# Optimization experiments

Hardware: AMD Instinct MI355X
Metric: run time of the kernel (lower is better)

Reference implementation:

```python
import jax, jax.numpy as jnp
import numpy as np

N, E, K, DEG = 150_000, 3_000_000, 4, 2
S = K * K  # 16 kernel weight matrices (kernel_size=4, dim=2)


def spline_coeffs(edge_attr):
    """Open quadratic B-spline basis, dim=2, kernel_size=4.
    Returns C [E, 16]: per-edge coefficient for each kernel weight index."""
    u = jnp.clip(edge_attr, 0.0, 1.0)
    v = u * (K - DEG)                      # [E,2], in [0, K-DEG]
    kv = jnp.floor(v)
    t = v - kv                             # [E,2] fractional part
    # quadratic uniform B-spline pieces
    b = jnp.stack([0.5 * (1.0 - t) ** 2,
                   -t * t + t + 0.5,
                   0.5 * t * t], axis=-1)  # [E,2,3]
    idx = jnp.clip(kv[..., None].astype(jnp.int32) + jnp.arange(3), 0, K - 1)  # [E,2,3]
    basis = (b[:, 0, :, None] * b[:, 1, None, :]).reshape(-1, 9)               # [E,9]
    widx = (idx[:, 0, :, None] + K * idx[:, 1, None, :]).reshape(-1, 9)        # [E,9]
    e_ar = jnp.arange(widx.shape[0])[:, None]
    C = jnp.zeros((widx.shape[0], S), basis.dtype).at[e_ar, widx].add(basis)   # [E,16]
    return C


def spline_conv(x, src, dst, C, weight, root, bias):
    # out_i = sum_{e: dst=i} sum_k C[e,k] * x[src[e]] @ W[k]  + x_i @ root + bias
    x_j = x[src]                                              # [E, in] gather
    out = x @ root + bias                                     # root_weight + bias
    for k in range(S):  # static small loop over 16 kernel matrices
        agg = jax.ops.segment_sum(C[:, k:k + 1] * x_j, dst, num_segments=N)  # [N,in]
        out = out + agg @ weight[k]
    return out


def batch_norm(x, gamma, beta, eps=1e-5):
    m = x.mean(axis=0)
    v = x.var(axis=0)  # biased, as torch BatchNorm1d training forward
    return (x - m) * jax.lax.rsqrt(v + eps) * gamma + beta


def setup_inputs() -> dict:
    key = jax.random.key(0)
    ks = jax.random.split(key, 18)
    f32 = jnp.float32
    return {
        "x": jax.random.normal(ks[0], (N, 1), f32),
        "edge_index": jax.random.randint(ks[1], (2, E), 0, N),
        "edge_attr": jax.random.uniform(ks[2], (E, 2), f32),
        "w1": jax.random.normal(ks[3], (S, 1, 32), f32) * 0.25,
        "root1": jax.random.normal(ks[4], (1, 32), f32) * 0.25,
        "b1": jnp.zeros((32,), f32),
        "gamma1": jnp.ones((32,), f32),
        "beta1": jnp.zeros((32,), f32),
        "w2": jax.random.normal(ks[5], (S, 32, 64), f32) * 0.05,
        "root2": jax.random.normal(ks[6], (32, 64), f32) * 0.05,
        "b2": jnp.zeros((64,), f32),
        "gamma2": jnp.ones((64,), f32),
        "beta2": jnp.zeros((64,), f32),
        "fc1_w": jax.random.normal(ks[7], (64, 128), f32) * 0.1,
        "fc1_b": jnp.zeros((128,), f32),
        "fc2_w": jax.random.normal(ks[8], (128, 1), f32) * 0.1,
        "fc2_b": jnp.zeros((1,), f32),
    }


def reference(x, edge_index, edge_attr, w1, root1, b1, gamma1, beta1,
              w2, root2, b2, gamma2, beta2, fc1_w, fc1_b, fc2_w, fc2_b):
    src, dst = edge_index[0], edge_index[1]
    C = spline_coeffs(edge_attr)            # shared by both conv layers
    h = spline_conv(x, src, dst, C, w1, root1, b1)
    h = jax.nn.elu(batch_norm(h, gamma1, beta1))
    h = spline_conv(h, src, dst, C, w2, root2, b2)
    h = jax.nn.elu(batch_norm(h, gamma2, beta2))  # [N,64]; flatten is identity
    h = jax.nn.elu(h @ fc1_w + fc1_b)
    return h @ fc2_w + fc2_b                 # [N,1]
```

## Files before the change

kernel.cpp:

```cpp
#include <hip/hip_runtime.h>
#include <hip/hip_fp16.h>
#include <math.h>


typedef _Float16 half8 __attribute__((ext_vector_type(8)));
typedef _Float16 half4 __attribute__((ext_vector_type(4)));
typedef float    f32x4 __attribute__((ext_vector_type(4)));
typedef int      iv4   __attribute__((ext_vector_type(4)));

#define ACHUNK 8192

__device__ __forceinline__ void bspline4(float a, float B[4]) {
    a = fminf(fmaxf(a, 0.f), 1.f);
    float v  = a * 2.0f;
    float kv = floorf(v);
    float t  = v - kv;
    int   ik = (int)kv;
    float b0 = 0.5f * (1.f - t) * (1.f - t);
    float b1 = (t - t * t) + 0.5f;
    float b2 = 0.5f * t * t;
    int c0 = ik;
    int c1 = ik + 1;
    int c2 = ik + 2; if (c2 > 3) c2 = 3;
#pragma unroll
    for (int j = 0; j < 4; ++j)
        B[j] = (c0 == j ? b0 : 0.f) + (c1 == j ? b1 : 0.f) + (c2 == j ? b2 : 0.f);
}

__device__ __forceinline__ float eluf(float x) {
    return x > 0.f ? x : expm1f(x);
}

__device__ __forceinline__ void unpack_basis(uint4 rec, float bu[4], float bv[4]) {
    float2 f01 = __half22float2(*(const __half2*)&rec.y);
    float2 f23 = __half22float2(*(const __half2*)&rec.z);
    float2 f45 = __half22float2(*(const __half2*)&rec.w);
    bu[0] = f01.x; bu[1] = f01.y; bu[2] = f23.x;
    bu[3] = 1.f - (bu[0] + bu[1] + bu[2]);
    bv[0] = f23.y; bv[1] = f45.x; bv[2] = f45.y;
    bv[3] = 1.f - (bv[0] + bv[1] + bv[2]);
}

__device__ __forceinline__ uint4 make_edge_rec(unsigned src, float u, float v) {
    float Bu[4], Bv[4];
    bspline4(u, Bu);
    bspline4(v, Bv);
    __half2 p01 = __floats2half2_rn(Bu[0], Bu[1]);
    __half2 p23 = __floats2half2_rn(Bu[2], Bv[0]);
    __half2 p45 = __floats2half2_rn(Bv[1], Bv[2]);
    uint4 rec;
    rec.x = src;
    rec.y = *(const unsigned*)&p01;
    rec.z = *(const unsigned*)&p23;
    rec.w = *(const unsigned*)&p45;
    return rec;
}


__global__ void kA1_hist(const int* __restrict__ dst, int E, int* __restrict__ cnt,
                         int nWG, int NBUK) {
    extern __shared__ int hist[];
    int wg = blockIdx.x, tid = threadIdx.x;
    for (int b = tid; b < NBUK; b += 256) hist[b] = 0;
    __syncthreads();
    int base = wg * ACHUNK;
    int end  = base + ACHUNK; if (end > E) end = E;
    for (int i = base + tid; i < end; i += 256)
        atomicAdd(&hist[dst[i] >> 8], 1);
    __syncthreads();
    for (int b = tid; b < NBUK; b += 256) cnt[b * nWG + wg] = hist[b];
}

__global__ void k_scan1(const int* __restrict__ in, int M,
                        int* __restrict__ outp, int* __restrict__ blockSums) {
    __shared__ int wsum[4];
    int tid  = threadIdx.x;
    int base = blockIdx.x * 1024 + tid * 4;
    int d0 = (base + 0) < M ? in[base + 0] : 0;
    int d1 = (base + 1) < M ? in[base + 1] : 0;
    int d2 = (base + 2) < M ? in[base + 2] : 0;
    int d3 = (base + 3) < M ? in[base + 3] : 0;
    int s4 = d0 + d1 + d2 + d3;
    int lane = tid & 63, wid = tid >> 6;
    int inc = s4;
#pragma unroll
    for (int off = 1; off < 64; off <<= 1) {
        int t = __shfl_up(inc, off);
        if (lane >= off) inc += t;
    }
    if (lane == 63) wsum[wid] = inc;
    __syncthreads();
    if (tid == 0) {
        int acc = 0;
#pragma unroll
        for (int w = 0; w < 4; ++w) { int t = wsum[w]; wsum[w] = acc; acc += t; }
    }
    __syncthreads();
    int ebase = wsum[wid] + inc - s4;
    if ((base + 0) < M) outp[base + 0] = ebase;
    if ((base + 1) < M) outp[base + 1] = ebase + d0;
    if ((base + 2) < M) outp[base + 2] = ebase + d0 + d1;
    if ((base + 3) < M) outp[base + 3] = ebase + d0 + d1 + d2;
    if (tid == 255) blockSums[blockIdx.x] = ebase + s4;
}

__global__ void k_scan2(const int* __restrict__ blockSums, int NB, int* __restrict__ blockOff) {
    __shared__ int sh[256];
    int tid = threadIdx.x;
    int own = (tid < NB) ? blockSums[tid] : 0;
    sh[tid] = own;
    __syncthreads();
    for (int off = 1; off < 256; off <<= 1) {
        int v = (tid >= off) ? sh[tid - off] : 0;
        __syncthreads();
        sh[tid] += v;
        __syncthreads();
    }
    if (tid < NB) blockOff[tid] = sh[tid] - own;
}

__global__ void k_scan3b(int* __restrict__ arr, const int* __restrict__ blockOff, int M) {
    int i = blockIdx.x * blockDim.x + threadIdx.x;
    if (i < M) arr[i] += blockOff[i >> 10];
}

__global__ __launch_bounds__(256) void kA2_fill(
    const int* __restrict__ ei, const float* __restrict__ attr, int E,
    const int* __restrict__ offs, int nWG, int NBUK,
    uint4* __restrict__ buf1, unsigned char* __restrict__ dl1) {
    extern __shared__ int lds[];
    int*            hist  = lds;
    int*            pref  = hist + NBUK;
    unsigned short* s2e   = (unsigned short*)(pref + NBUK);
    unsigned short* bslot = s2e + ACHUNK;
    __shared__ int wsum[4];
    int wg = blockIdx.x, tid = threadIdx.x;
    int base  = wg * ACHUNK;
    int csize = E - base; if (csize > ACHUNK) csize = ACHUNK;

    for (int b = tid; b < NBUK; b += 256) hist[b] = 0;
    __syncthreads();

    int ranks[32];
#pragma unroll
    for (int k = 0; k < 32; ++k) {
        int i = tid + (k << 8);
        if (i < csize) {
            int b = ei[E + base + i] >> 8;
            ranks[k] = atomicAdd(&hist[b], 1);
        }
    }
    __syncthreads();

    int IT = (NBUK + 255) >> 8;
    int b0 = tid * IT;
    int lsum = 0;
    for (int k = 0; k < IT; ++k) {
        int b = b0 + k;
        if (b < NBUK) lsum += hist[b];
    }
    int lane = tid & 63, wid = tid >> 6;
    int inc = lsum;
#pragma unroll
    for (int off = 1; off < 64; off <<= 1) {
        int t = __shfl_up(inc, off);
        if (lane >= off) inc += t;
    }
    if (lane == 63) wsum[wid] = inc;
    __syncthreads();
    if (tid == 0) {
        int acc = 0;
#pragma unroll
        for (int w = 0; w < 4; ++w) { int t = wsum[w]; wsum[w] = acc; acc += t; }
    }
    __syncthreads();
    int run = wsum[wid] + inc - lsum;
    for (int k = 0; k < IT; ++k) {
        int b = b0 + k;
        if (b < NBUK) { pref[b] = run; run += hist[b]; }
    }
    __syncthreads();

#pragma unroll
    for (int k = 0; k < 32; ++k) {
        int i = tid + (k << 8);
        if (i < csize) {
            int b = ei[E + base + i] >> 8;
            int s = pref[b] + ranks[k];
            s2e[s]   = (unsigned short)i;
            bslot[s] = (unsigned short)b;
        }
    }
    __syncthreads();

    for (int s = tid; s < csize; s += 256) {
        int i  = s2e[s];
        int b  = bslot[s];
        int gi = base + i;
        int gpos = offs[b * nWG + wg] + (s - pref[b]);
        int d  = ei[E + gi];
        uint4 rec = make_edge_rec((unsigned)ei[gi], attr[2 * gi], attr[2 * gi + 1]);
        buf1[gpos] = rec;
        dl1[gpos]  = (unsigned char)(d & 255);
    }
}


__global__ __launch_bounds__(256) void kB_sort(
    const uint4* __restrict__ buf1, const unsigned char* __restrict__ dl1,
    const int* __restrict__ off, int nWG, int NBUK, int N, int E,
    uint4* __restrict__ edges, int* __restrict__ rowptr) {
    __shared__ int hist[256], pref[256], curs[256];
    __shared__ int sbase, ssize;
    int b = blockIdx.x, tid = threadIdx.x;
    if (tid == 0) {
        int s  = off[b * nWG];
        int e2 = (b + 1 < NBUK) ? off[(b + 1) * nWG] : E;
        sbase = s; ssize = e2 - s;
    }
    hist[tid] = 0;
    __syncthreads();
    int base = sbase, size = ssize;
    for (int i = tid; i < size; i += 256) atomicAdd(&hist[dl1[base + i]], 1);
    __syncthreads();
    if (tid == 0) {
        int acc = 0;
        for (int j = 0; j < 256; ++j) { pref[j] = acc; acc += hist[j]; }
    }
    __syncthreads();
    curs[tid] = pref[tid];
    int node = b * 256 + tid;
    if (node < N) rowptr[node] = base + pref[tid];
    if (b == NBUK - 1 && tid == 0) rowptr[N] = E;
    __syncthreads();
    for (int i = tid; i < size; i += 256) {
        int p = atomicAdd(&curs[dl1[base + i]], 1);
        edges[base + p] = buf1[base + i];
    }
}


__global__ void k_w2pack(const float* __restrict__ w2, const float* __restrict__ root2,
                         _Float16* __restrict__ w2f) {
    int f = blockIdx.x * blockDim.x + threadIdx.x;
    int stride = gridDim.x * blockDim.x;
    for (; f < 34816; f += stride) {
        int j = f & 7, l = (f >> 3) & 63, t = (f >> 9) & 3;
        int o = t * 16 + (l & 15);
        float v;
        if (f < 32768) {
            int s = f >> 11;
            int p = s * 32 + ((l >> 4) << 3) + j;
            int ch = p >> 4, k = p & 15;
            v = w2[(k * 32 + ch) * 64 + o];
        } else {
            int ci = ((l >> 4) << 3) + j;
            v = root2[ci * 64 + o];
        }
        w2f[f] = (_Float16)v;
    }
}


__global__ void k_fcpack(const float* __restrict__ fc1w, _Float16* __restrict__ fc1wf) {
    int f = blockIdx.x * blockDim.x + threadIdx.x;
    if (f >= 8192) return;
    int j = f & 7, l = (f >> 3) & 63, t = (f >> 9) & 7, s = f >> 12;
    int k = s * 32 + ((l >> 4) << 3) + j;
    int o = t * 16 + (l & 15);
    fc1wf[f] = (_Float16)fc1w[k * 128 + o];
}


__global__ void k_conv1(const float* __restrict__ x, const int* __restrict__ rowptr,
                        const uint4* __restrict__ edges,
                        const float* __restrict__ w1, const float* __restrict__ root1,
                        const float* __restrict__ b1, _Float16* __restrict__ h1h, int N) {
    __shared__ float w1s[16 * 32];
    __shared__ float r1s[32], b1s[32];
    int tid = threadIdx.x;
    for (int i = tid; i < 512; i += blockDim.x) w1s[i] = w1[i];
    if (tid < 32) { r1s[tid] = root1[tid]; b1s[tid] = b1[tid]; }
    __syncthreads();
    int n = blockIdx.x * blockDim.x + tid;
    if (n >= N) return;
    float agg[16] = {};
    int s = rowptr[n], e = rowptr[n + 1];

#define P1(rec, xs) { \
    float bu[4], bv[4]; \
    unpack_basis(rec, bu, bv); \
    float t0 = (xs) * bv[0], t1 = (xs) * bv[1], t2 = (xs) * bv[2], t3 = (xs) * bv[3]; \
    agg[0]  += bu[0] * t0; agg[1]  += bu[1] * t0; agg[2]  += bu[2] * t0; agg[3]  += bu[3] * t0; \
    agg[4]  += bu[0] * t1; agg[5]  += bu[1] * t1; agg[6]  += bu[2] * t1; agg[7]  += bu[3] * t1; \
    agg[8]  += bu[0] * t2; agg[9]  += bu[1] * t2; agg[10] += bu[2] * t2; agg[11] += bu[3] * t2; \
    agg[12] += bu[0] * t3; agg[13] += bu[1] * t3; agg[14] += bu[2] * t3; agg[15] += bu[3] * t3; }

    int j = s;
    for (; j + 3 < e; j += 4) {
        uint4 r0 = edges[j], r1 = edges[j + 1], r2 = edges[j + 2], r3 = edges[j + 3];
        float x0 = x[r0.x], x1 = x[r1.x], x2 = x[r2.x], x3 = x[r3.x];
        P1(r0, x0); P1(r1, x1); P1(r2, x2); P1(r3, x3);
    }
    for (; j < e; ++j) {
        uint4 r = edges[j];
        float xs = x[r.x];
        P1(r, xs);
    }
#undef P1

    float xn = x[n];
    _Float16* hp = h1h + (size_t)n * 32;
#pragma unroll
    for (int o8 = 0; o8 < 4; ++o8) {
        half8 hv;
#pragma unroll
        for (int oo = 0; oo < 8; ++oo) {
            int o = o8 * 8 + oo;
            float acc = b1s[o] + xn * r1s[o];
#pragma unroll
            for (int k = 0; k < 16; ++k) acc += agg[k] * w1s[k * 32 + o];
            hv[oo] = (_Float16)acc;
        }
        *(half8*)(hp + o8 * 8) = hv;
    }
}


template <int C>
__global__ void k_bnstath(const _Float16* __restrict__ h, int N, double* __restrict__ sums) {
    __shared__ float sh1[C], sh2[C];
    int tid  = blockIdx.x * blockDim.x + threadIdx.x;
    int c    = tid & (C - 1);
    int row  = tid / C;
    int rstr = (gridDim.x * blockDim.x) / C;
    float s1 = 0.f, s2 = 0.f;
    for (int r = row; r < N; r += rstr) {
        float v = (float)h[(size_t)r * C + c];
        s1 += v; s2 += v * v;
    }
    if (threadIdx.x < C) { sh1[threadIdx.x] = 0.f; sh2[threadIdx.x] = 0.f; }
    __syncthreads();
    atomicAdd(&sh1[c], s1);
    atomicAdd(&sh2[c], s2);
    __syncthreads();
    if (threadIdx.x < C) {
        atomicAdd(&sums[threadIdx.x],     (double)sh1[threadIdx.x]);
        atomicAdd(&sums[C + threadIdx.x], (double)sh2[threadIdx.x]);
    }
}

__global__ void k_bnfinal(const double* __restrict__ sums, const float* __restrict__ gamma,
                          const float* __restrict__ beta, int C, int N, float* __restrict__ scsh) {
    int c = threadIdx.x;
    if (c < C) {
        double m   = sums[c] / (double)N;
        double var = sums[C + c] / (double)N - m * m;
        float vpe  = (float)var + 1e-5f;
        float sc   = gamma[c] / sqrtf(vpe);
        scsh[c]     = sc;
        scsh[C + c] = beta[c] - (float)m * sc;
    }
}

__global__ void k_bnelu32h(_Float16* __restrict__ hh, int N, const float* __restrict__ scsh) {
    int total = N * 4;
    int i = blockIdx.x * blockDim.x + threadIdx.x;
    int stride = gridDim.x * blockDim.x;
    for (; i < total; i += stride) {
        half8 v = *(half8*)(hh + (size_t)i * 8);
        int c0 = (i * 8) & 31;
        half8 r;
#pragma unroll
        for (int j = 0; j < 8; ++j)
            r[j] = (_Float16)eluf((float)v[j] * scsh[c0 + j] + scsh[32 + c0 + j]);
        *(half8*)(hh + (size_t)i * 8) = r;
    }
}


__global__ __launch_bounds__(256) void k_ag2(
    const _Float16* __restrict__ h1h, const int* __restrict__ rowptr,
    const uint4* __restrict__ edges, const _Float16* __restrict__ w2f,
    const float* __restrict__ b2, _Float16* __restrict__ out2h, int N) {
    __shared__ __align__(16) _Float16 aggL[16][520];
    __shared__ __align__(16) _Float16 basisL[4][16][72];
    __shared__ __align__(16) int      srcL[4][64];
    int tid = threadIdx.x, l = tid & 63, w = tid >> 6;
    int g = l >> 4, m = l & 15;
    int n0 = blockIdx.x * 16;

    for (int q = 0; q < 4; ++q) {
        int row = w * 4 + q;
        int n = n0 + row;
        if (n < N) {
            int s = __builtin_amdgcn_readfirstlane(rowptr[n]);
            int e = __builtin_amdgcn_readfirstlane(rowptr[n + 1]);
            f32x4 C0 = {0.f, 0.f, 0.f, 0.f}, C1 = C0;
            for (int t = s; t < e; t += 64) {
                int eg = t + l;
                bool act = eg < e;
                uint4 rec = edges[act ? eg : e - 1];
                srcL[w][l] = act ? (int)rec.x : 0;
                float bu[4], bv[4];
                unpack_basis(rec, bu, bv);
#pragma unroll
                for (int kv = 0; kv < 4; ++kv)
#pragma unroll
                    for (int ku = 0; ku < 4; ++ku)
                        basisL[w][kv * 4 + ku][l] = (_Float16)(bu[ku] * bv[kv]);
                int rem = e - t;
#pragma unroll
                for (int kh = 0; kh < 2; ++kh) {
                    if (kh == 1 && rem <= 32) break;
                    int ebase = kh * 32 + g * 8;
                    half8 a = *(const half8*)&basisL[w][m][ebase];
                    iv4 sA = *(const iv4*)&srcL[w][ebase];
                    iv4 sB = *(const iv4*)&srcL[w][ebase + 4];
                    half8 b0, b1;
#pragma unroll
                    for (int j = 0; j < 8; ++j) {
                        int sj = (j < 4) ? sA[j] : sB[j - 4];
                        bool aj = (t + ebase + j) < e;
                        _Float16 v0 = h1h[(size_t)sj * 32 + m];
                        _Float16 v1 = h1h[(size_t)sj * 32 + 16 + m];
                        b0[j] = aj ? v0 : (_Float16)0.f;
                        b1[j] = aj ? v1 : (_Float16)0.f;
                    }
                    C0 = __builtin_amdgcn_mfma_f32_16x16x32_f16(a, b0, C0, 0, 0, 0);
                    C1 = __builtin_amdgcn_mfma_f32_16x16x32_f16(a, b1, C1, 0, 0, 0);
                }
            }
            half4 c0, c1;
#pragma unroll
            for (int r = 0; r < 4; ++r) { c0[r] = (_Float16)C0[r]; c1[r] = (_Float16)C1[r]; }
            *(half4*)&aggL[row][m * 16 + g * 4]        = c0;
            *(half4*)&aggL[row][(16 + m) * 16 + g * 4] = c1;
        }
    }
    __syncthreads();

    f32x4 acc = {0.f, 0.f, 0.f, 0.f};
#pragma unroll
    for (int s = 0; s < 16; ++s) {
        half8 a = *(const half8*)&aggL[m][s * 32 + g * 8];
        half8 b = *(const half8*)&w2f[(size_t)(((s * 4 + w) * 64) + l) * 8];
        acc = __builtin_amdgcn_mfma_f32_16x16x32_f16(a, b, acc, 0, 0, 0);
    }
    {
        int nn = n0 + m; if (nn > N - 1) nn = N - 1;
        half8 a = *(const half8*)&h1h[(size_t)nn * 32 + g * 8];
        half8 b = *(const half8*)&w2f[(size_t)(((64 + w) * 64) + l) * 8];
        acc = __builtin_amdgcn_mfma_f32_16x16x32_f16(a, b, acc, 0, 0, 0);
    }
    int o = w * 16 + m;
    float bb = b2[o];
#pragma unroll
    for (int r = 0; r < 4; ++r) {
        int node = n0 + g * 4 + r;
        if (node < N) out2h[(size_t)node * 64 + o] = (_Float16)(acc[r] + bb);
    }
}


__global__ __launch_bounds__(256) void k_fcm(
    const _Float16* __restrict__ out2h, const _Float16* __restrict__ fc1wf,
    const float* __restrict__ scsh, const float* __restrict__ fc1b,
    const float* __restrict__ fc2w, const float* __restrict__ fc2b,
    float* __restrict__ out, int N, int ntiles) {
    __shared__ _Float16 fw[8192];
    __shared__ float scs[64], shs[64], b1s[128], w2sv[128];
    int tid = threadIdx.x;
    {
        const uint4* s4 = (const uint4*)fc1wf;
        uint4* d4 = (uint4*)fw;
        for (int i = tid; i < 1024; i += 256) d4[i] = s4[i];
    }
    if (tid < 128) { b1s[tid] = fc1b[tid]; w2sv[tid] = fc2w[tid]; }
    if (tid < 64)  { scs[tid] = scsh[tid]; shs[tid] = scsh[64 + tid]; }
    __syncthreads();
    const half8* bp = (const half8*)fw;
    int l = tid & 63, w = tid >> 6;
    int g = l >> 4, m = l & 15, klo = g * 8;
    float f2b = fc2b[0];
    for (int tile = blockIdx.x * 4 + w; tile < ntiles; tile += gridDim.x * 4) {
        int base = tile * 16;
        int arow = base + m; if (arow > N - 1) arow = N - 1;
        const half8* hp = (const half8*)(out2h + (size_t)arow * 64 + klo);
        half8 r0 = hp[0];
        half8 r1 = hp[4];
        half8 a0, a1;
#pragma unroll
        for (int j = 0; j < 8; ++j) {
            int c0 = klo + j, c1 = 32 + klo + j;
            a0[j] = (_Float16)eluf((float)r0[j] * scs[c0] + shs[c0]);
            a1[j] = (_Float16)eluf((float)r1[j] * scs[c1] + shs[c1]);
        }
        f32x4 acc[8];
#pragma unroll
        for (int t = 0; t < 8; ++t) {
            f32x4 z = {0.f, 0.f, 0.f, 0.f};
            acc[t] = __builtin_amdgcn_mfma_f32_16x16x32_f16(a0, bp[t * 64 + l], z, 0, 0, 0);
            acc[t] = __builtin_amdgcn_mfma_f32_16x16x32_f16(a1, bp[(8 + t) * 64 + l], acc[t], 0, 0, 0);
        }
#pragma unroll
        for (int r = 0; r < 4; ++r) {
            float sum = 0.f;
#pragma unroll
            for (int t = 0; t < 8; ++t) {
                int o = t * 16 + m;
                sum += eluf(acc[t][r] + b1s[o]) * w2sv[o];
            }
            sum += __shfl_xor(sum, 1);
            sum += __shfl_xor(sum, 2);
            sum += __shfl_xor(sum, 4);
            sum += __shfl_xor(sum, 8);
            int node = base + g * 4 + r;
            if (m == 0 && node < N) out[node] = sum + f2b;
        }
    }
}


extern "C" void kernel_launch(void* const* d_in, const int* in_sizes, int n_in,
                              void* d_out, int out_size, void* d_ws, size_t ws_size,
                              hipStream_t stream) {
    const float* x     = (const float*)d_in[0];
    const int*   ei    = (const int*)  d_in[1];
    const float* attr  = (const float*)d_in[2];
    const float* w1    = (const float*)d_in[3];
    const float* root1 = (const float*)d_in[4];
    const float* b1    = (const float*)d_in[5];
    const float* g1    = (const float*)d_in[6];
    const float* be1   = (const float*)d_in[7];
    const float* w2    = (const float*)d_in[8];
    const float* root2 = (const float*)d_in[9];
    const float* b2    = (const float*)d_in[10];
    const float* g2    = (const float*)d_in[11];
    const float* be2   = (const float*)d_in[12];
    const float* fc1w  = (const float*)d_in[13];
    const float* fc1b  = (const float*)d_in[14];
    const float* fc2w  = (const float*)d_in[15];
    const float* fc2b  = (const float*)d_in[16];
    float* out = (float*)d_out;

    int N = in_sizes[0];
    int E = in_sizes[1] / 2;

    int nWG  = (E + ACHUNK - 1) / ACHUNK;
    int NBUK = (N + 255) >> 8;
    int M    = NBUK * nWG;

    char* ws = (char*)d_ws;
    size_t off = 0;
    auto alloc = [&](size_t bytes) -> void* {
        void* p = ws + off;
        off = (off + bytes + 255) & ~(size_t)255;
        return p;
    };
    int*      rowptr    = (int*)     alloc((size_t)(N + 1) * 4);
    int*      blockSums = (int*)     alloc(1024 * 4);
    int*      blockOff  = (int*)     alloc(1024 * 4);
    double*   bnsum1    = (double*)  alloc(128 * 8);
    double*   bnsum2    = (double*)  alloc(128 * 8);
    float*    scsh1     = (float*)   alloc(64 * 4);
    float*    scsh2     = (float*)   alloc(128 * 4);
    _Float16* w2f       = (_Float16*)alloc(34816 * 2);
    _Float16* fc1wf     = (_Float16*)alloc(8192 * 2);
    int*      cnt       = (int*)     alloc((size_t)M * 4);
    int*      offs      = (int*)     alloc((size_t)M * 4);
    uint4*    edges     = (uint4*)   alloc((size_t)E * 16);
    size_t    Roff      = off;
    _Float16* h1h       = (_Float16*)alloc((size_t)N * 32 * 2);
    _Float16* out2h     = (_Float16*)alloc((size_t)N * 64 * 2);
    uint4*         buf1 = (uint4*)(ws + Roff);
    unsigned char* dl1  = (unsigned char*)(ws + Roff + (size_t)E * 16);
    (void)n_in; (void)out_size; (void)ws_size;

    hipMemsetAsync(bnsum1, 0, 128 * 8, stream);
    hipMemsetAsync(bnsum2, 0, 128 * 8, stream);

    size_t ldsA1 = (size_t)NBUK * 4;
    size_t ldsA2 = (size_t)NBUK * 8 + (size_t)ACHUNK * 4;
    int NBs = (M + 1023) / 1024;

    k_w2pack<<<136, 256, 0, stream>>>(w2, root2, w2f);
    k_fcpack<<<32, 256, 0, stream>>>(fc1w, fc1wf);
    kA1_hist<<<nWG, 256, ldsA1, stream>>>(ei + E, E, cnt, nWG, NBUK);
    k_scan1<<<NBs, 256, 0, stream>>>(cnt, M, offs, blockSums);
    k_scan2<<<1, 256, 0, stream>>>(blockSums, NBs, blockOff);
    k_scan3b<<<(M + 255) / 256, 256, 0, stream>>>(offs, blockOff, M);
    kA2_fill<<<nWG, 256, ldsA2, stream>>>(ei, attr, E, offs, nWG, NBUK, buf1, dl1);
    kB_sort<<<NBUK, 256, 0, stream>>>(buf1, dl1, offs, nWG, NBUK, N, E, edges, rowptr);

    k_conv1<<<(N + 255) / 256, 256, 0, stream>>>(x, rowptr, edges, w1, root1, b1, h1h, N);
    k_bnstath<32><<<256, 256, 0, stream>>>(h1h, N, bnsum1);
    k_bnfinal<<<1, 64, 0, stream>>>(bnsum1, g1, be1, 32, N, scsh1);
    k_bnelu32h<<<1024, 256, 0, stream>>>(h1h, N, scsh1);

    k_ag2<<<(N + 15) / 16, 256, 0, stream>>>(h1h, rowptr, edges, w2f, b2, out2h, N);

    k_bnstath<64><<<256, 256, 0, stream>>>(out2h, N, bnsum2);
    k_bnfinal<<<1, 64, 0, stream>>>(bnsum2, g2, be2, 64, N, scsh2);

    int ntilesF = (N + 15) / 16;
    int gridF = (ntilesF + 3) / 4; if (gridF > 2344) gridF = 2344;
    k_fcm<<<gridF, 256, 0, stream>>>(out2h, fc1wf, scsh2, fc1b, fc2w, fc2b, out, N, ntilesF);
}
```

Baseline: 378.2 us.

## Stage coalesced edge source and attr in LDS during bucket fill; halve chunk

The bucket-scatter fill kernel now reads each edge's source index and attributes in original (coalesced) order and stages them in LDS. Attributes are stored there as packed fp16. The final scatter loop then reads from LDS instead of doing random global gathers per sorted slot. Destination values are kept in registers, the prefix is written in place over the histogram, and slot metadata is packed into one 32-bit word. The chunk size is halved, which doubles the number of workgroups and count entries, so the second-level scan now handles two block sums per thread. Rounding edge attributes to fp16 before building the spline record may slightly change the coefficients.

```diff
diff --git a/kernel.cpp b/kernel.cpp
--- a/kernel.cpp
+++ b/kernel.cpp
@@ -8,7 +8,7 @@
 typedef float    f32x4 __attribute__((ext_vector_type(4)));
 typedef int      iv4   __attribute__((ext_vector_type(4)));
 
-#define ACHUNK 8192
+#define ACHUNK 4096
 
 __device__ __forceinline__ void bspline4(float a, float B[4]) {
     a = fminf(fmaxf(a, 0.f), 1.f);
@@ -107,8 +107,11 @@
 __global__ void k_scan2(const int* __restrict__ blockSums, int NB, int* __restrict__ blockOff) {
     __shared__ int sh[256];
     int tid = threadIdx.x;
-    int own = (tid < NB) ? blockSums[tid] : 0;
-    sh[tid] = own;
+    int i0 = 2 * tid, i1 = 2 * tid + 1;
+    int a = (i0 < NB) ? blockSums[i0] : 0;
+    int b = (i1 < NB) ? blockSums[i1] : 0;
+    int p = a + b;
+    sh[tid] = p;
     __syncthreads();
     for (int off = 1; off < 256; off <<= 1) {
         int v = (tid >= off) ? sh[tid - off] : 0;
@@ -116,7 +119,9 @@
         sh[tid] += v;
         __syncthreads();
     }
-    if (tid < NB) blockOff[tid] = sh[tid] - own;
+    int excl = sh[tid] - p;
+    if (i0 < NB) blockOff[i0] = excl;
+    if (i1 < NB) blockOff[i1] = excl + a;
 }
 
 __global__ void k_scan3b(int* __restrict__ arr, const int* __restrict__ blockOff, int M) {
@@ -129,10 +134,10 @@
     const int* __restrict__ offs, int nWG, int NBUK,
     uint4* __restrict__ buf1, unsigned char* __restrict__ dl1) {
     extern __shared__ int lds[];
-    int*            hist  = lds;
-    int*            pref  = hist + NBUK;
-    unsigned short* s2e   = (unsigned short*)(pref + NBUK);
-    unsigned short* bslot = s2e + ACHUNK;
+    int*      hist  = lds;
+    int*      srcS  = hist + NBUK;
+    unsigned* attrS = (unsigned*)(srcS + ACHUNK);
+    unsigned* meta  = attrS + ACHUNK;
     __shared__ int wsum[4];
     int wg = blockIdx.x, tid = threadIdx.x;
     int base  = wg * ACHUNK;
@@ -141,13 +146,14 @@
     for (int b = tid; b < NBUK; b += 256) hist[b] = 0;
     __syncthreads();
 
-    int ranks[32];
-#pragma unroll
-    for (int k = 0; k < 32; ++k) {
+    int dArr[16], ranks[16];
+#pragma unroll
+    for (int k = 0; k < 16; ++k) {
         int i = tid + (k << 8);
         if (i < csize) {
-            int b = ei[E + base + i] >> 8;
-            ranks[k] = atomicAdd(&hist[b], 1);
+            int d = ei[E + base + i];
+            dArr[k]  = d;
+            ranks[k] = atomicAdd(&hist[d >> 8], 1);
         }
     }
     __syncthreads();
@@ -177,31 +183,36 @@
     int run = wsum[wid] + inc - lsum;
     for (int k = 0; k < IT; ++k) {
         int b = b0 + k;
-        if (b < NBUK) { pref[b] = run; run += hist[b]; }
-    }
-    __syncthreads();
-
-#pragma unroll
-    for (int k = 0; k < 32; ++k) {
+        if (b < NBUK) { int h = hist[b]; hist[b] = run; run += h; }
+    }
+    __syncthreads();
+
+#pragma unroll
+    for (int k = 0; k < 16; ++k) {
         int i = tid + (k << 8);
         if (i < csize) {
-            int b = ei[E + base + i] >> 8;
-            int s = pref[b] + ranks[k];
-            s2e[s]   = (unsigned short)i;
-            bslot[s] = (unsigned short)b;
+            int gi = base + i;
+            int d  = dArr[k];
+            int b  = d >> 8;
+            int s  = hist[b] + ranks[k];
+            meta[s] = (unsigned)i | ((unsigned)b << 12) | ((unsigned)(d & 255) << 22);
+            srcS[i] = ei[gi];
+            __half2 uv = __floats2half2_rn(attr[2 * gi], attr[2 * gi + 1]);
+            attrS[i] = *(const unsigned*)&uv;
         }
     }
     __syncthreads();
 
     for (int s = tid; s < csize; s += 256) {
-        int i  = s2e[s];
-        int b  = bslot[s];
-        int gi = base + i;
-        int gpos = offs[b * nWG + wg] + (s - pref[b]);
-        int d  = ei[E + gi];
-        uint4 rec = make_edge_rec((unsigned)ei[gi], attr[2 * gi], attr[2 * gi + 1]);
+        unsigned mt = meta[s];
+        int i = mt & 4095;
+        int b = (mt >> 12) & 1023;
+        unsigned av = attrS[i];
+        float2 uv = __half22float2(*(const __half2*)&av);
+        uint4 rec = make_edge_rec((unsigned)srcS[i], uv.x, uv.y);
+        int gpos = offs[b * nWG + wg] + (s - hist[b]);
         buf1[gpos] = rec;
-        dl1[gpos]  = (unsigned char)(d & 255);
+        dl1[gpos]  = (unsigned char)(mt >> 22);
     }
 }
 
@@ -581,7 +592,7 @@
     hipMemsetAsync(bnsum2, 0, 128 * 8, stream);
 
     size_t ldsA1 = (size_t)NBUK * 4;
-    size_t ldsA2 = (size_t)NBUK * 8 + (size_t)ACHUNK * 4;
+    size_t ldsA2 = (size_t)NBUK * 4 + (size_t)ACHUNK * 12;
     int NBs = (M + 1023) / 1024;
 
     k_w2pack<<<136, 256, 0, stream>>>(w2, root2, w2f);
```

New measurement: 316.4 us. -16.3%, faster.
